# Kernel tuning notes

Measured on AMD Instinct MI355X. Metric: run time of the kernel, lower is better.

## Reference

```python
import jax, jax.numpy as jnp
import numpy as np

B, S, D, F = 4, 2048, 1024, 4096

def setup_inputs() -> dict:
    key = jax.random.key(0)
    ks = jax.random.split(key, 6)
    return {
        "x": jax.random.normal(ks[0], (B, S, D), jnp.float32),
        "Qw": jax.random.normal(ks[1], (D, D), jnp.float32) / 40,
        "Kw": jax.random.normal(ks[2], (D, D), jnp.float32) / 40,
        "Vw": jax.random.normal(ks[3], (D, D), jnp.float32) / 40,
        "w1": jax.random.normal(ks[4], (D, F), jnp.float32) / 40,
        "b1": jnp.zeros((F,), jnp.float32),
        "w2": jax.random.normal(ks[5], (F, D), jnp.float32) / 40,
        "b2": jnp.zeros((D,), jnp.float32),
        "gamma1": jnp.ones((D,), jnp.float32),
        "beta1": jnp.zeros((D,), jnp.float32),
        "gamma2": jnp.ones((D,), jnp.float32),
        "beta2": jnp.zeros((D,), jnp.float32),
    }

def _layernorm(x, gamma, beta):
    num = x - jnp.mean(x, axis=-1, keepdims=True)
    den = jnp.sqrt(jnp.var(x, axis=-1, keepdims=True) + 1e-05)
    return gamma * (num / den) + beta

def _attention(x, Qw, Kw, Vw):
    Q, K, V = x @ Qw, x @ Kw, x @ Vw
    d = x.shape[-1]
    s = x.shape[-2]
    mask = jnp.where(jnp.tril(jnp.ones((s, s))) == 0, -jnp.inf, 0.0)
    scores = Q @ jnp.swapaxes(K, -1, -2) / jnp.sqrt(d) + mask
    return jax.nn.softmax(scores, axis=-1) @ V

def reference(x, Qw, Kw, Vw, w1, b1, w2, b2, gamma1, beta1, gamma2, beta2):
    x = x + _attention(_layernorm(x, gamma1, beta1), Qw, Kw, Vw)
    h = _layernorm(x, gamma2, beta2)
    x = x + (jax.nn.relu(h @ w1 + b1) @ w2 + b2)
    return x
```

## Files before the change

### kernel.cpp

```cpp
#include <hip/hip_runtime.h>
#include <hip/hip_bf16.h>

#define B_ 4
#define S_ 2048
#define D_ 1024
#define F_ 4096

typedef short bf16x8 __attribute__((ext_vector_type(8)));
typedef float f32x4 __attribute__((ext_vector_type(4)));

static __device__ __forceinline__ unsigned short f2bf(float f) {
    union { float f; unsigned int u; } v; v.f = f;
    unsigned int u = v.u + 0x7FFF + ((v.u >> 16) & 1);
    return (unsigned short)(u >> 16);
}
static __device__ __forceinline__ float bf2f(unsigned short u) {
    union { unsigned int u; float f; } v; v.u = ((unsigned int)u) << 16;
    return v.f;
}

typedef const __attribute__((address_space(1))) unsigned int* gp_t;
typedef __attribute__((address_space(3))) unsigned int* lp_t;
static __device__ __forceinline__ void gld16(const unsigned short* g, unsigned short* l) {
    __builtin_amdgcn_global_load_lds((gp_t)g, (lp_t)l, 16, 0, 0);
}

#define WAIT_VM8()   __builtin_amdgcn_s_waitcnt(0x0F78)
#define WAIT_VM6()   __builtin_amdgcn_s_waitcnt(0x0F76)
#define WAIT_VM4()   __builtin_amdgcn_s_waitcnt(0x0F74)
#define WAIT_VM0()   __builtin_amdgcn_s_waitcnt(0x0F70)
#define WAIT_LGKM0() __builtin_amdgcn_s_waitcnt(0xC07F)

__global__ __launch_bounds__(256) void k_transpose_f32_bf16(
    const float* __restrict__ in, unsigned short* __restrict__ out, int R, int C) {
    __shared__ float t[32][33];
    int c0 = blockIdx.x * 32, r0 = blockIdx.y * 32;
    int x = threadIdx.x, y = threadIdx.y;
#pragma unroll
    for (int i = 0; i < 4; i++)
        t[y + 8 * i][x] = in[(size_t)(r0 + y + 8 * i) * C + c0 + x];
    __syncthreads();
#pragma unroll
    for (int i = 0; i < 4; i++)
        out[(size_t)(c0 + y + 8 * i) * R + r0 + x] = f2bf(t[x][y + 8 * i]);
}

__global__ __launch_bounds__(256) void k_transpose_w3(
    const float* __restrict__ Qw, const float* __restrict__ Kw, const float* __restrict__ Vw,
    unsigned short* __restrict__ out) {
    __shared__ float t[32][33];
    int z = blockIdx.z;
    const float* in = (z == 0) ? Qw : (z == 1) ? Kw : Vw;
    out += (size_t)z * D_ * D_;
    int c0 = blockIdx.x * 32, r0 = blockIdx.y * 32;
    int x = threadIdx.x, y = threadIdx.y;
#pragma unroll
    for (int i = 0; i < 4; i++)
        t[y + 8 * i][x] = in[(size_t)(r0 + y + 8 * i) * D_ + c0 + x];
    __syncthreads();
#pragma unroll
    for (int i = 0; i < 4; i++)
        out[(size_t)(c0 + y + 8 * i) * D_ + r0 + x] = f2bf(t[x][y + 8 * i]);
}

__global__ __launch_bounds__(256) void k_transpose_bf16(
    const unsigned short* __restrict__ in, unsigned short* __restrict__ out,
    int ldin, int ldout, long long szin, long long szout) {
    __shared__ unsigned short t[32][33];
    in += (long long)blockIdx.z * szin;
    out += (long long)blockIdx.z * szout;
    int c0 = blockIdx.x * 32, r0 = blockIdx.y * 32;
    int x = threadIdx.x, y = threadIdx.y;
#pragma unroll
    for (int i = 0; i < 4; i++)
        t[y + 8 * i][x] = in[(size_t)(r0 + y + 8 * i) * ldin + c0 + x];
    __syncthreads();
#pragma unroll
    for (int i = 0; i < 4; i++)
        out[(size_t)(c0 + y + 8 * i) * ldout + r0 + x] = t[x][y + 8 * i];
}

__global__ __launch_bounds__(256) void k_layernorm(
    const float* __restrict__ x, const float* __restrict__ gamma,
    const float* __restrict__ beta, unsigned short* __restrict__ out) {
    int row = blockIdx.x;
    int t = threadIdx.x;
    const float* xr = x + (size_t)row * D_;
    float4 v = ((const float4*)xr)[t];
    float s = v.x + v.y + v.z + v.w;
    float q = v.x * v.x + v.y * v.y + v.z * v.z + v.w * v.w;
#pragma unroll
    for (int off = 32; off; off >>= 1) {
        s += __shfl_down(s, off);
        q += __shfl_down(q, off);
    }
    __shared__ float ls[4], lq[4];
    int wv = t >> 6;
    if ((t & 63) == 0) { ls[wv] = s; lq[wv] = q; }
    __syncthreads();
    if (t == 0) {
        float S = ls[0] + ls[1] + ls[2] + ls[3];
        float Q = lq[0] + lq[1] + lq[2] + lq[3];
        float mean = S * (1.0f / D_);
        float var = Q * (1.0f / D_) - mean * mean;
        ls[0] = mean; lq[0] = rsqrtf(var + 1e-5f);
    }
    __syncthreads();
    float mean = ls[0], rstd = lq[0];
    float4 g = ((const float4*)gamma)[t];
    float4 b = ((const float4*)beta)[t];
    ushort4 o;
    o.x = f2bf(g.x * (v.x - mean) * rstd + b.x);
    o.y = f2bf(g.y * (v.y - mean) * rstd + b.y);
    o.z = f2bf(g.z * (v.z - mean) * rstd + b.z);
    o.w = f2bf(g.w * (v.w - mean) * rstd + b.w);
    ((ushort4*)(out + (size_t)row * D_))[t] = o;
}

__global__ __launch_bounds__(256) void k_softmax(unsigned short* __restrict__ sp) {
    int r = blockIdx.x;
    int i = r & (S_ - 1);
    unsigned short* row = sp + (size_t)r * S_;
    int t = threadIdx.x;
    int valid = i + 1;
    float vals[8];
    float mx = -1e30f;
#pragma unroll
    for (int k = 0; k < 8; k++) {
        int j = t + k * 256;
        vals[k] = (j < valid) ? bf2f(row[j]) : -1e30f;
        mx = fmaxf(mx, vals[k]);
    }
#pragma unroll
    for (int off = 32; off; off >>= 1) mx = fmaxf(mx, __shfl_xor(mx, off));
    __shared__ float red[4];
    if ((t & 63) == 0) red[t >> 6] = mx;
    __syncthreads();
    mx = fmaxf(fmaxf(red[0], red[1]), fmaxf(red[2], red[3]));
    __syncthreads();
    float e[8];
    float sum = 0.f;
#pragma unroll
    for (int k = 0; k < 8; k++) {
        int j = t + k * 256;
        e[k] = (j < valid) ? __expf(vals[k] - mx) : 0.f;
        sum += e[k];
    }
#pragma unroll
    for (int off = 32; off; off >>= 1) sum += __shfl_xor(sum, off);
    if ((t & 63) == 0) red[t >> 6] = sum;
    __syncthreads();
    sum = red[0] + red[1] + red[2] + red[3];
    float inv = 1.0f / sum;
#pragma unroll
    for (int k = 0; k < 8; k++) {
        int j = t + k * 256;
        row[j] = f2bf(e[k] * inv);
    }
}

template <int EPI>
__global__ __launch_bounds__(256) void k_gemm_bt(
    const unsigned short* __restrict__ A, const unsigned short* __restrict__ Bt,
    void* __restrict__ Cv, const float* __restrict__ bias, const float* __restrict__ res,
    int K, int lda, int ldb, int ldc,
    long long sA, long long sB, long long sC, float scale, int klimit, int swz) {
    int bn, bm, z;
    if (swz > 0) {
        int GN = gridDim.x, GM = gridDim.y;
        int L = blockIdx.x + GN * (blockIdx.y + GM * blockIdx.z);
        int rows = gridDim.y * gridDim.z;
        int xcd = L & 7;
        int s = L >> 3;
        int bng = GN / swz;
        int rpg = rows * swz / 8;
        int xg = xcd % swz, yg = xcd / swz;
        int bnl = s % bng;
        int rl = s / bng;
        int row = yg * rpg + rl;
        bn = xg * bng + bnl;
        bm = row % GM;
        z = row / GM;
    } else {
        bn = blockIdx.x; bm = blockIdx.y; z = blockIdx.z;
    }
    if (EPI == 1 && bn > bm) return;
    A += (long long)z * sA;
    Bt += (long long)z * sB;
    long long coff = (long long)z * sC;
    float* Cf = (float*)Cv;
    unsigned short* Cb = (unsigned short*)Cv;

    __shared__ unsigned short As[2][2][128 * 32];
    __shared__ unsigned short Bs[2][2][128 * 32];

    int t = threadIdx.x;
    int l = t & 63, w = t >> 6;
    int wm = (w & 1) * 64, wn = (w >> 1) * 64;
    int lr = l & 15, lq = l >> 4;

    f32x4 acc[4][4];
#pragma unroll
    for (int i = 0; i < 4; i++)
#pragma unroll
        for (int j = 0; j < 4; j++) acc[i][j] = (f32x4){0.f, 0.f, 0.f, 0.f};

    int kend = K;
    if (klimit) { int ke = (bm + 1) * 128; kend = ke < K ? ke : K; }

    int sr = l >> 2;
    int sc = (l & 3) * 8;
    const unsigned short* gA0 = A + (size_t)(bm * 128 + w * 32 + sr) * lda + sc;
    const unsigned short* gA1 = gA0 + (size_t)16 * lda;
    const unsigned short* gB0 = Bt + (size_t)(bn * 128 + w * 32 + sr) * ldb + sc;
    const unsigned short* gB1 = gB0 + (size_t)16 * ldb;

    auto stage = [&](int buf, int k0) {
#pragma unroll
        for (int kc = 0; kc < 2; kc++) {
            int kk = k0 + kc * 32;
            gld16(gA0 + kk, &As[buf][kc][(w * 32) * 32]);
            gld16(gA1 + kk, &As[buf][kc][(w * 32 + 16) * 32]);
            gld16(gB0 + kk, &Bs[buf][kc][(w * 32) * 32]);
            gld16(gB1 + kk, &Bs[buf][kc][(w * 32 + 16) * 32]);
        }
    };

    int NB = kend >> 6;
    stage(0, 0);
    for (int it = 0; it < NB; it++) {
        int cur = it & 1;
        if (it + 1 < NB) {
            stage(1 - cur, (it + 1) * 64);
            WAIT_VM8();
        } else {
            WAIT_VM0();
        }
        __builtin_amdgcn_s_barrier();
#pragma unroll
        for (int kc = 0; kc < 2; kc++) {
            bf16x8 af[4], bf[4];
#pragma unroll
            for (int i = 0; i < 4; i++)
                af[i] = *(const bf16x8*)(&As[cur][kc][(wm + i * 16 + lr) * 32 + lq * 8]);
#pragma unroll
            for (int j = 0; j < 4; j++)
                bf[j] = *(const bf16x8*)(&Bs[cur][kc][(wn + j * 16 + lr) * 32 + lq * 8]);
#pragma unroll
            for (int i = 0; i < 4; i++)
#pragma unroll
                for (int j = 0; j < 4; j++)
                    acc[i][j] = __builtin_amdgcn_mfma_f32_16x16x32_bf16(af[i], bf[j], acc[i][j], 0, 0, 0);
        }
        __builtin_amdgcn_s_barrier();
    }

#pragma unroll
    for (int i = 0; i < 4; i++) {
        int mbase = bm * 128 + wm + i * 16 + lq * 4;
#pragma unroll
        for (int j = 0; j < 4; j++) {
            int n = bn * 128 + wn + j * 16 + lr;
#pragma unroll
            for (int r = 0; r < 4; r++) {
                int m = mbase + r;
                float v = acc[i][j][r];
                long long idx = coff + (long long)m * ldc + n;
                if (EPI == 0) {
                    Cb[idx] = f2bf(v);
                } else if (EPI == 1) {
                    Cb[idx] = f2bf(v * scale);
                } else if (EPI == 2) {
                    Cf[idx] = v + res[idx];
                } else if (EPI == 3) {
                    float u = v + bias[n];
                    Cb[idx] = f2bf(u > 0.f ? u : 0.f);
                } else {
                    Cf[idx] = v + bias[n] + res[idx];
                }
            }
        }
    }
}

template <int EPI>
__global__ __launch_bounds__(512, 2) void k_gemm256(
    const unsigned short* __restrict__ A, const unsigned short* __restrict__ Bt,
    void* __restrict__ Cv, const float* __restrict__ bias, const float* __restrict__ res,
    int K, int lda, int ldb, int ldc,
    long long sA, long long sB, long long sC, float scale, int klimit) {
    int bn = blockIdx.x, bm = blockIdx.y, z = blockIdx.z;
    if (EPI == 1 && bn > bm) return;
    A += (long long)z * sA;
    Bt += (long long)z * sB;
    long long coff = (long long)z * sC;
    float* Cf = (float*)Cv;
    unsigned short* Cb = (unsigned short*)Cv;

    __shared__ unsigned short As[2][2][128 * 64];
    __shared__ unsigned short Bs[2][2][128 * 64];

    int t = threadIdx.x;
    int l = t & 63, w = t >> 6;
    int wmh = w >> 2;
    int wnh = (w >> 1) & 1;
    int bnl = (w & 1) * 64;
    int lr = l & 15, lq = l >> 4;
    int rx = (lr & 7) << 3;
    int c0 = lq * 8;

    f32x4 acc[8][4];
#pragma unroll
    for (int i = 0; i < 8; i++)
#pragma unroll
        for (int j = 0; j < 4; j++) acc[i][j] = (f32x4){0.f, 0.f, 0.f, 0.f};

    int kend = K;
    if (klimit) { int ke = (bm + 1) * 256; kend = ke < K ? ke : K; }
    int NB = kend >> 6;

    int grow = l >> 3;
    int gcol = ((l & 7) * 8) ^ (((l >> 3) & 7) << 3);
    const unsigned short* gA = A + (size_t)(bm * 256 + w * 16 + grow) * lda + gcol;
    const unsigned short* gB = Bt + (size_t)(bn * 256 + w * 16 + grow) * ldb + gcol;

    auto stageA = [&](int buf, int half, int k0) {
        const unsigned short* g = gA + (size_t)(half * 128) * lda + k0;
        unsigned short* s = &As[buf][half][(w * 16) * 64];
        gld16(g, s);
        gld16(g + (size_t)8 * lda, s + 8 * 64);
    };
    auto stageB = [&](int buf, int half, int k0) {
        const unsigned short* g = gB + (size_t)(half * 128) * ldb + k0;
        unsigned short* s = &Bs[buf][half][(w * 16) * 64];
        gld16(g, s);
        gld16(g + (size_t)8 * ldb, s + 8 * 64);
    };

    stageA(0, 0, 0); stageA(0, 1, 0);
    stageB(0, 0, 0); stageB(0, 1, 0);
    int kp = (NB > 1) ? 64 : 0;
    stageB(1, 0, kp); stageB(1, 1, kp); stageA(1, 0, kp);
    WAIT_VM6();
    __builtin_amdgcn_s_barrier();

    bf16x8 aF0[2][4], aF1[2][4], bF[2][4];

    for (int j = 0; j < NB; j++) {
        int b = j & 1;
        int k1 = ((j + 1 < NB) ? (j + 1) : (NB - 1)) << 6;
        int k2 = ((j + 2 < NB) ? (j + 2) : (NB - 1)) << 6;
        const unsigned short* Ah = &As[b][wmh][0];
        const unsigned short* Bh = &Bs[b][wnh][0];

#pragma unroll
        for (int kc = 0; kc < 2; kc++) {
#pragma unroll
            for (int f = 0; f < 4; f++)
                bF[kc][f] = *(const bf16x8*)(Bh + (bnl + f * 16 + lr) * 64 + ((kc * 32 + c0) ^ rx));
#pragma unroll
            for (int f = 0; f < 4; f++)
                aF0[kc][f] = *(const bf16x8*)(Ah + (f * 16 + lr) * 64 + ((kc * 32 + c0) ^ rx));
        }
        stageA(b ^ 1, 1, k1);
        __builtin_amdgcn_s_barrier();
        __builtin_amdgcn_s_setprio(1);
#pragma unroll
        for (int kc = 0; kc < 2; kc++)
#pragma unroll
            for (int i = 0; i < 4; i++)
#pragma unroll
                for (int jn = 0; jn < 2; jn++)
                    acc[i][jn] = __builtin_amdgcn_mfma_f32_16x16x32_bf16(
                        aF0[kc][i], bF[kc][jn], acc[i][jn], 0, 0, 0);
        __builtin_amdgcn_s_setprio(0);
        __builtin_amdgcn_s_barrier();

#pragma unroll
        for (int kc = 0; kc < 2; kc++)
#pragma unroll
            for (int f = 0; f < 4; f++)
                aF1[kc][f] = *(const bf16x8*)(Ah + (64 + f * 16 + lr) * 64 + ((kc * 32 + c0) ^ rx));
        stageB(b, 0, k2);
        __builtin_amdgcn_s_barrier();
        __builtin_amdgcn_s_setprio(1);
#pragma unroll
        for (int kc = 0; kc < 2; kc++)
#pragma unroll
            for (int i = 0; i < 4; i++)
#pragma unroll
                for (int jn = 0; jn < 2; jn++)
                    acc[4 + i][jn] = __builtin_amdgcn_mfma_f32_16x16x32_bf16(
                        aF1[kc][i], bF[kc][jn], acc[4 + i][jn], 0, 0, 0);
        __builtin_amdgcn_s_setprio(0);
        __builtin_amdgcn_s_barrier();

        stageB(b, 1, k2);
        __builtin_amdgcn_s_barrier();
        __builtin_amdgcn_s_setprio(1);
#pragma unroll
        for (int kc = 0; kc < 2; kc++)
#pragma unroll
            for (int i = 0; i < 4; i++)
#pragma unroll
                for (int jn = 0; jn < 2; jn++)
                    acc[4 + i][2 + jn] = __builtin_amdgcn_mfma_f32_16x16x32_bf16(
                        aF1[kc][i], bF[kc][2 + jn], acc[4 + i][2 + jn], 0, 0, 0);
        __builtin_amdgcn_s_setprio(0);
        __builtin_amdgcn_s_barrier();

        stageA(b, 0, k2);
        WAIT_VM6();
        __builtin_amdgcn_s_barrier();
        __builtin_amdgcn_s_setprio(1);
#pragma unroll
        for (int kc = 0; kc < 2; kc++)
#pragma unroll
            for (int i = 0; i < 4; i++)
#pragma unroll
                for (int jn = 0; jn < 2; jn++)
                    acc[i][2 + jn] = __builtin_amdgcn_mfma_f32_16x16x32_bf16(
                        aF0[kc][i], bF[kc][2 + jn], acc[i][2 + jn], 0, 0, 0);
        __builtin_amdgcn_s_setprio(0);
        __builtin_amdgcn_s_barrier();
    }
    WAIT_VM0();

#pragma unroll
    for (int i = 0; i < 8; i++) {
        int mbase = bm * 256 + wmh * 128 + i * 16 + lq * 4;
#pragma unroll
        for (int jn = 0; jn < 4; jn++) {
            int n = bn * 256 + (w & 3) * 64 + jn * 16 + lr;
#pragma unroll
            for (int r = 0; r < 4; r++) {
                int m = mbase + r;
                float v = acc[i][jn][r];
                long long idx = coff + (long long)m * ldc + n;
                if (EPI == 0) {
                    Cb[idx] = f2bf(v);
                } else if (EPI == 1) {
                    Cb[idx] = f2bf(v * scale);
                } else if (EPI == 2) {
                    Cf[idx] = v + res[idx];
                } else if (EPI == 3) {
                    float u = v + bias[n];
                    Cb[idx] = f2bf(u > 0.f ? u : 0.f);
                } else {
                    Cf[idx] = v + bias[n] + res[idx];
                }
            }
        }
    }
}

template <int EPI>
__global__ __launch_bounds__(512, 2) void k_gemm_b128(
    const unsigned short* __restrict__ A, const unsigned short* __restrict__ Bt,
    void* __restrict__ Cv, const float* __restrict__ bias, const float* __restrict__ res,
    int K, int lda, int ldb, int ldc,
    long long sA, long long sB, long long sC, float scale, int klimit) {
    int bn = blockIdx.x, bm = blockIdx.y, z = blockIdx.z;
    A += (long long)z * sA;
    Bt += (long long)z * sB;
    long long coff = (long long)z * sC;
    float* Cf = (float*)Cv;
    unsigned short* Cb = (unsigned short*)Cv;

    __shared__ unsigned short As[2][2][128 * 64];
    __shared__ unsigned short Bs[2][128 * 64];

    int t = threadIdx.x;
    int l = t & 63, w = t >> 6;
    int wq = w >> 1;
    int wnn = w & 1;
    int ah = wq >> 1;
    int mb = (wq & 1) * 64;
    int bnl = wnn * 64;
    int lr = l & 15, lq = l >> 4;
    int rx = (lr & 7) << 3;
    int c0 = lq * 8;

    f32x4 acc[4][4];
#pragma unroll
    for (int i = 0; i < 4; i++)
#pragma unroll
        for (int j = 0; j < 4; j++) acc[i][j] = (f32x4){0.f, 0.f, 0.f, 0.f};

    int kend = K;
    if (klimit) { int ke = (bm + 1) * 256; kend = ke < K ? ke : K; }
    int NB = kend >> 6;

    int grow = l >> 3;
    int gcol = ((l & 7) * 8) ^ (((l >> 3) & 7) << 3);
    const unsigned short* gA = A + (size_t)(bm * 256 + w * 16 + grow) * lda + gcol;
    const unsigned short* gB = Bt + (size_t)(bn * 128 + w * 16 + grow) * ldb + gcol;

    auto stageA = [&](int buf, int half, int k0) {
        const unsigned short* g = gA + (size_t)(half * 128) * lda + k0;
        unsigned short* s = &As[buf][half][(w * 16) * 64];
        gld16(g, s);
        gld16(g + (size_t)8 * lda, s + 8 * 64);
    };
    auto stageB = [&](int buf, int k0) {
        const unsigned short* g = gB + k0;
        unsigned short* s = &Bs[buf][(w * 16) * 64];
        gld16(g, s);
        gld16(g + (size_t)8 * ldb, s + 8 * 64);
    };

    stageA(0, 0, 0); stageA(0, 1, 0); stageB(0, 0);
    if (NB > 1) {
        stageB(1, 64); stageA(1, 0, 64);
        WAIT_VM4();
    } else {
        WAIT_VM0();
    }
    __builtin_amdgcn_s_barrier();

    bf16x8 aF0[2][2], aF1[2][2], bF[2][4];

    for (int j = 0; j < NB; j++) {
        int b = j & 1;
        const unsigned short* Ah = &As[b][ah][0];
        const unsigned short* Bh = &Bs[b][0];

#pragma unroll
        for (int kc = 0; kc < 2; kc++) {
#pragma unroll
            for (int f = 0; f < 4; f++)
                bF[kc][f] = *(const bf16x8*)(Bh + (bnl + f * 16 + lr) * 64 + ((kc * 32 + c0) ^ rx));
#pragma unroll
            for (int f = 0; f < 2; f++)
                aF0[kc][f] = *(const bf16x8*)(Ah + (mb + f * 16 + lr) * 64 + ((kc * 32 + c0) ^ rx));
        }
        if (j + 1 < NB) stageA(b ^ 1, 1, (j + 1) << 6);
        WAIT_LGKM0();
        __builtin_amdgcn_s_barrier();
        __builtin_amdgcn_s_setprio(1);
#pragma unroll
        for (int kc = 0; kc < 2; kc++)
#pragma unroll
            for (int i = 0; i < 2; i++)
#pragma unroll
                for (int jn = 0; jn < 2; jn++)
                    acc[i][jn] = __builtin_amdgcn_mfma_f32_16x16x32_bf16(
                        aF0[kc][i], bF[kc][jn], acc[i][jn], 0, 0, 0);
        __builtin_amdgcn_s_setprio(0);
        __builtin_amdgcn_s_barrier();

#pragma unroll
        for (int kc = 0; kc < 2; kc++)
#pragma unroll
            for (int f = 0; f < 2; f++)
                aF1[kc][f] = *(const bf16x8*)(Ah + (mb + 32 + f * 16 + lr) * 64 + ((kc * 32 + c0) ^ rx));
        if (j + 2 < NB) stageB(b, (j + 2) << 6);
        __builtin_amdgcn_s_barrier();
        __builtin_amdgcn_s_setprio(1);
#pragma unroll
        for (int kc = 0; kc < 2; kc++)
#pragma unroll
            for (int i = 0; i < 2; i++)
#pragma unroll
                for (int jn = 0; jn < 4; jn++)
                    acc[2 + i][jn] = __builtin_amdgcn_mfma_f32_16x16x32_bf16(
                        aF1[kc][i], bF[kc][jn], acc[2 + i][jn], 0, 0, 0);
        __builtin_amdgcn_s_setprio(0);
        __builtin_amdgcn_s_barrier();

        if (j + 2 < NB) {
            stageA(b, 0, (j + 2) << 6);
            WAIT_VM4();
        } else {
            WAIT_VM0();
        }
        __builtin_amdgcn_s_barrier();
        __builtin_amdgcn_s_setprio(1);
#pragma unroll
        for (int kc = 0; kc < 2; kc++)
#pragma unroll
            for (int i = 0; i < 2; i++)
#pragma unroll
                for (int jn = 0; jn < 2; jn++)
                    acc[i][2 + jn] = __builtin_amdgcn_mfma_f32_16x16x32_bf16(
                        aF0[kc][i], bF[kc][2 + jn], acc[i][2 + jn], 0, 0, 0);
        __builtin_amdgcn_s_setprio(0);
        __builtin_amdgcn_s_barrier();
    }
    WAIT_VM0();

#pragma unroll
    for (int i = 0; i < 4; i++) {
        int mbase = bm * 256 + ah * 128 + mb + i * 16 + lq * 4;
#pragma unroll
        for (int jn = 0; jn < 4; jn++) {
            int n = bn * 128 + bnl + jn * 16 + lr;
#pragma unroll
            for (int r = 0; r < 4; r++) {
                int m = mbase + r;
                float v = acc[i][jn][r];
                long long idx = coff + (long long)m * ldc + n;
                if (EPI == 0) {
                    Cb[idx] = f2bf(v);
                } else if (EPI == 1) {
                    Cb[idx] = f2bf(v * scale);
                } else if (EPI == 2) {
                    Cf[idx] = v + res[idx];
                } else if (EPI == 3) {
                    float u = v + bias[n];
                    Cb[idx] = f2bf(u > 0.f ? u : 0.f);
                } else {
                    Cf[idx] = v + bias[n] + res[idx];
                }
            }
        }
    }
}

extern "C" void kernel_launch(void* const* d_in, const int* in_sizes, int n_in,
                              void* d_out, int out_size, void* d_ws, size_t ws_size,
                              hipStream_t stream) {
    const float* x      = (const float*)d_in[0];
    const float* Qw     = (const float*)d_in[1];
    const float* Kw     = (const float*)d_in[2];
    const float* Vw     = (const float*)d_in[3];
    const float* w1     = (const float*)d_in[4];
    const float* b1     = (const float*)d_in[5];
    const float* w2     = (const float*)d_in[6];
    const float* b2     = (const float*)d_in[7];
    const float* gamma1 = (const float*)d_in[8];
    const float* beta1  = (const float*)d_in[9];
    const float* gamma2 = (const float*)d_in[10];
    const float* beta2  = (const float*)d_in[11];
    float* out = (float*)d_out;

    char* ws = (char*)d_ws;
    size_t off = 0;
    auto alloc = [&](size_t bytes) -> void* {
        void* p = ws + off;
        off += (bytes + 255) & ~(size_t)255;
        return p;
    };
    const size_t MN = (size_t)B_ * S_ * D_;
    unsigned short* xn     = (unsigned short*)alloc(MN * 2);
    unsigned short* scoreP = (unsigned short*)alloc((size_t)B_ * S_ * S_ * 2);
    unsigned short* qkv    = (unsigned short*)alloc((size_t)B_ * S_ * 3072 * 2);
    unsigned short* VT     = (unsigned short*)alloc(MN * 2);
    unsigned short* QKVwT  = (unsigned short*)alloc((size_t)3 * D_ * D_ * 2);
    unsigned short* w1T    = (unsigned short*)alloc((size_t)D_ * F_ * 2);
    unsigned short* w2T    = (unsigned short*)alloc((size_t)F_ * D_ * 2);
    unsigned short* mid = qkv;

    dim3 tb(32, 8);
    k_transpose_w3<<<dim3(D_ / 32, D_ / 32, 3), tb, 0, stream>>>(Qw, Kw, Vw, QKVwT);
    k_transpose_f32_bf16<<<dim3(F_ / 32, D_ / 32), tb, 0, stream>>>(w1, w1T, D_, F_);
    k_transpose_f32_bf16<<<dim3(D_ / 32, F_ / 32), tb, 0, stream>>>(w2, w2T, F_, D_);

    k_layernorm<<<B_ * S_, 256, 0, stream>>>(x, gamma1, beta1, xn);

    const int Mtok = B_ * S_;
    k_gemm256<0><<<dim3(3072 / 256, Mtok / 256), 512, 0, stream>>>(
        xn, QKVwT, qkv, nullptr, nullptr, D_, D_, D_, 3072, 0, 0, 0, 1.f, 0);

    k_transpose_bf16<<<dim3(D_ / 32, S_ / 32, B_), tb, 0, stream>>>(
        qkv + 2048, VT, 3072, S_, (long long)S_ * 3072, (long long)D_ * S_);

    k_gemm256<1><<<dim3(S_ / 256, S_ / 256, B_), 512, 0, stream>>>(
        qkv, qkv + 1024, scoreP, nullptr, nullptr, D_, 3072, 3072, S_,
        (long long)S_ * 3072, (long long)S_ * 3072, (long long)S_ * S_, 0.03125f, 0);

    k_softmax<<<B_ * S_, 256, 0, stream>>>(scoreP);

    k_gemm_bt<2><<<dim3(D_ / 128, S_ / 128, B_), 256, 0, stream>>>(
        scoreP, VT, out, nullptr, x, S_, S_, S_, D_,
        (long long)S_ * S_, (long long)D_ * S_, (long long)S_ * D_, 1.f, 1, 2);

    k_layernorm<<<B_ * S_, 256, 0, stream>>>(out, gamma2, beta2, xn);

    k_gemm256<3><<<dim3(F_ / 256, Mtok / 256), 512, 0, stream>>>(
        xn, w1T, mid, b1, nullptr, D_, D_, D_, F_, 0, 0, 0, 1.f, 0);

    k_gemm_b128<4><<<dim3(D_ / 128, Mtok / 256), 512, 0, stream>>>(
        mid, w2T, out, b2, out, F_, F_, F_, D_, 0, 0, 0, 1.f, 0);
}
```

Before: 493.9 us.

## Rework FFN down-proj GEMM pipeline with split B staging and XCD-aware block swizzle

The 256x128 FFN down-projection GEMM now stages the B tile in two 64-row halves issued at separate phases. It adds a fourth MFMA phase per k-step so loads interleave more evenly with compute. Tail-iteration branches become clamped, redundant loads, and the explicit LDS waitcnt before the first barrier is dropped. Block indices are remapped so consecutive blocks landing on the same XCD share A rows, aiming for better L2 reuse, at the cost of extra barriers and redundant final loads.

```diff
diff --git a/kernel.cpp b/kernel.cpp
--- a/kernel.cpp
+++ b/kernel.cpp
@@ -29,7 +29,6 @@
 #define WAIT_VM6()   __builtin_amdgcn_s_waitcnt(0x0F76)
 #define WAIT_VM4()   __builtin_amdgcn_s_waitcnt(0x0F74)
 #define WAIT_VM0()   __builtin_amdgcn_s_waitcnt(0x0F70)
-#define WAIT_LGKM0() __builtin_amdgcn_s_waitcnt(0xC07F)
 
 __global__ __launch_bounds__(256) void k_transpose_f32_bf16(
     const float* __restrict__ in, unsigned short* __restrict__ out, int R, int C) {
@@ -455,12 +454,21 @@
 }
 
 template <int EPI>
-__global__ __launch_bounds__(512, 2) void k_gemm_b128(
+__global__ __launch_bounds__(512, 2) void k_gemm_n128(
     const unsigned short* __restrict__ A, const unsigned short* __restrict__ Bt,
     void* __restrict__ Cv, const float* __restrict__ bias, const float* __restrict__ res,
     int K, int lda, int ldb, int ldc,
-    long long sA, long long sB, long long sC, float scale, int klimit) {
-    int bn = blockIdx.x, bm = blockIdx.y, z = blockIdx.z;
+    long long sA, long long sB, long long sC, float scale, int swz) {
+    int bn, bm, z = blockIdx.z;
+    if (swz) {
+        int L = blockIdx.x + gridDim.x * blockIdx.y;
+        int xcd = L & 7;
+        int s = L >> 3;
+        bn = s % gridDim.x;
+        bm = xcd * (gridDim.y >> 3) + s / gridDim.x;
+    } else {
+        bn = blockIdx.x; bm = blockIdx.y;
+    }
     A += (long long)z * sA;
     Bt += (long long)z * sB;
     long long coff = (long long)z * sC;
@@ -468,7 +476,7 @@
     unsigned short* Cb = (unsigned short*)Cv;
 
     __shared__ unsigned short As[2][2][128 * 64];
-    __shared__ unsigned short Bs[2][128 * 64];
+    __shared__ unsigned short Bs[2][2][64 * 64];
 
     int t = threadIdx.x;
     int l = t & 63, w = t >> 6;
@@ -476,7 +484,6 @@
     int wnn = w & 1;
     int ah = wq >> 1;
     int mb = (wq & 1) * 64;
-    int bnl = wnn * 64;
     int lr = l & 15, lq = l >> 4;
     int rx = (lr & 7) << 3;
     int c0 = lq * 8;
@@ -487,14 +494,12 @@
 #pragma unroll
         for (int j = 0; j < 4; j++) acc[i][j] = (f32x4){0.f, 0.f, 0.f, 0.f};
 
-    int kend = K;
-    if (klimit) { int ke = (bm + 1) * 256; kend = ke < K ? ke : K; }
-    int NB = kend >> 6;
+    int NB = K >> 6;
 
     int grow = l >> 3;
     int gcol = ((l & 7) * 8) ^ (((l >> 3) & 7) << 3);
     const unsigned short* gA = A + (size_t)(bm * 256 + w * 16 + grow) * lda + gcol;
-    const unsigned short* gB = Bt + (size_t)(bn * 128 + w * 16 + grow) * ldb + gcol;
+    const unsigned short* gB = Bt + (size_t)(bn * 128 + w * 8 + grow) * ldb + gcol;
 
     auto stageA = [&](int buf, int half, int k0) {
         const unsigned short* g = gA + (size_t)(half * 128) * lda + k0;
@@ -502,40 +507,37 @@
         gld16(g, s);
         gld16(g + (size_t)8 * lda, s + 8 * 64);
     };
-    auto stageB = [&](int buf, int k0) {
-        const unsigned short* g = gB + k0;
-        unsigned short* s = &Bs[buf][(w * 16) * 64];
-        gld16(g, s);
-        gld16(g + (size_t)8 * ldb, s + 8 * 64);
+    auto stageB = [&](int buf, int half, int k0) {
+        const unsigned short* g = gB + (size_t)(half * 64) * ldb + k0;
+        gld16(g, &Bs[buf][half][(w * 8) * 64]);
     };
 
-    stageA(0, 0, 0); stageA(0, 1, 0); stageB(0, 0);
-    if (NB > 1) {
-        stageB(1, 64); stageA(1, 0, 64);
-        WAIT_VM4();
-    } else {
-        WAIT_VM0();
-    }
+    stageA(0, 0, 0); stageA(0, 1, 0);
+    stageB(0, 0, 0); stageB(0, 1, 0);
+    int kp = (NB > 1) ? 64 : 0;
+    stageB(1, 0, kp); stageB(1, 1, kp); stageA(1, 0, kp);
+    WAIT_VM4();
     __builtin_amdgcn_s_barrier();
 
     bf16x8 aF0[2][2], aF1[2][2], bF[2][4];
 
     for (int j = 0; j < NB; j++) {
         int b = j & 1;
+        int k1 = ((j + 1 < NB) ? (j + 1) : (NB - 1)) << 6;
+        int k2 = ((j + 2 < NB) ? (j + 2) : (NB - 1)) << 6;
         const unsigned short* Ah = &As[b][ah][0];
-        const unsigned short* Bh = &Bs[b][0];
+        const unsigned short* Bh = &Bs[b][wnn][0];
 
 #pragma unroll
         for (int kc = 0; kc < 2; kc++) {
 #pragma unroll
             for (int f = 0; f < 4; f++)
-                bF[kc][f] = *(const bf16x8*)(Bh + (bnl + f * 16 + lr) * 64 + ((kc * 32 + c0) ^ rx));
+                bF[kc][f] = *(const bf16x8*)(Bh + (f * 16 + lr) * 64 + ((kc * 32 + c0) ^ rx));
 #pragma unroll
             for (int f = 0; f < 2; f++)
                 aF0[kc][f] = *(const bf16x8*)(Ah + (mb + f * 16 + lr) * 64 + ((kc * 32 + c0) ^ rx));
         }
-        if (j + 1 < NB) stageA(b ^ 1, 1, (j + 1) << 6);
-        WAIT_LGKM0();
+        stageA(b ^ 1, 1, k1);
         __builtin_amdgcn_s_barrier();
         __builtin_amdgcn_s_setprio(1);
 #pragma unroll
@@ -554,7 +556,7 @@
 #pragma unroll
             for (int f = 0; f < 2; f++)
                 aF1[kc][f] = *(const bf16x8*)(Ah + (mb + 32 + f * 16 + lr) * 64 + ((kc * 32 + c0) ^ rx));
-        if (j + 2 < NB) stageB(b, (j + 2) << 6);
+        stageB(b, 0, k2);
         __builtin_amdgcn_s_barrier();
         __builtin_amdgcn_s_setprio(1);
 #pragma unroll
@@ -562,18 +564,28 @@
 #pragma unroll
             for (int i = 0; i < 2; i++)
 #pragma unroll
-                for (int jn = 0; jn < 4; jn++)
+                for (int jn = 0; jn < 2; jn++)
                     acc[2 + i][jn] = __builtin_amdgcn_mfma_f32_16x16x32_bf16(
                         aF1[kc][i], bF[kc][jn], acc[2 + i][jn], 0, 0, 0);
         __builtin_amdgcn_s_setprio(0);
         __builtin_amdgcn_s_barrier();
 
-        if (j + 2 < NB) {
-            stageA(b, 0, (j + 2) << 6);
-            WAIT_VM4();
-        } else {
-            WAIT_VM0();
-        }
+        stageB(b, 1, k2);
+        __builtin_amdgcn_s_barrier();
+        __builtin_amdgcn_s_setprio(1);
+#pragma unroll
+        for (int kc = 0; kc < 2; kc++)
+#pragma unroll
+            for (int i = 0; i < 2; i++)
+#pragma unroll
+                for (int jn = 0; jn < 2; jn++)
+                    acc[2 + i][2 + jn] = __builtin_amdgcn_mfma_f32_16x16x32_bf16(
+                        aF1[kc][i], bF[kc][2 + jn], acc[2 + i][2 + jn], 0, 0, 0);
+        __builtin_amdgcn_s_setprio(0);
+        __builtin_amdgcn_s_barrier();
+
+        stageA(b, 0, k2);
+        WAIT_VM4();
         __builtin_amdgcn_s_barrier();
         __builtin_amdgcn_s_setprio(1);
 #pragma unroll
@@ -594,7 +606,7 @@
         int mbase = bm * 256 + ah * 128 + mb + i * 16 + lq * 4;
 #pragma unroll
         for (int jn = 0; jn < 4; jn++) {
-            int n = bn * 128 + bnl + jn * 16 + lr;
+            int n = bn * 128 + wnn * 64 + jn * 16 + lr;
 #pragma unroll
             for (int r = 0; r < 4; r++) {
                 int m = mbase + r;
@@ -680,6 +692,6 @@
     k_gemm256<3><<<dim3(F_ / 256, Mtok / 256), 512, 0, stream>>>(
         xn, w1T, mid, b1, nullptr, D_, D_, D_, F_, 0, 0, 0, 1.f, 0);
 
-    k_gemm_b128<4><<<dim3(D_ / 128, Mtok / 256), 512, 0, stream>>>(
-        mid, w2T, out, b2, out, F_, F_, F_, D_, 0, 0, 0, 1.f, 0);
-}
+    k_gemm_n128<4><<<dim3(D_ / 128, Mtok / 256), 512, 0, stream>>>(
+        mid, w2T, out, b2, out, F_, F_, F_, D_, 0, 0, 0, 1.f, 1);
+}
```

Measured after the change: 479.2 us. 1.03x faster.
